# Kernel tuning notes

Measured on AMD Instinct MI355X. Metric: run time of the kernel, lower is better.

The kernel has to match this reference:

```python
import jax, jax.numpy as jnp
import numpy as np
from jax.scipy.special import erfinv

NEAR, FAR = 2.0, 6.0
NUM_COARSE, NUM_FINE = 128, 128
MAX_IPE_DEG = 16
REG_RED = 1.0            # cfg.train_params.reg_reduction_factor
SMOOTH = 2.0             # cfg.train_params.gaussian_smooth_factor
SQRT_2_OVER_PI = 0.7978845608028654


def approximate_cdf(x):
    # tanh approximation of the standard normal CDF (as in DDNeRF)
    return 0.5 * (1.0 + jnp.tanh(SQRT_2_OVER_PI * (x + 0.044715 * x ** 3)))


def cast_rays(t_vals, ro, rd, rr):
    # conical frustum -> diagonal gaussian (mip-NeRF)
    t0, t1 = t_vals[..., :-1], t_vals[..., 1:]
    c = 0.5 * (t0 + t1)
    d = 0.5 * (t1 - t0)
    denom = 3.0 * c ** 2 + d ** 2
    t_mean = c + (2.0 * c * d ** 2) / denom
    t_var = d ** 2 / 3.0 - (4.0 / 15.0) * (d ** 4 * (12.0 * c ** 2 - d ** 2)) / denom ** 2
    r_var = rr ** 2 * (c ** 2 / 4.0 + (5.0 / 12.0) * d ** 2 - (4.0 / 15.0) * d ** 4 / denom)
    mean = ro[..., None, :] + rd[..., None, :] * t_mean[..., None]          # [N,S,3]
    d2 = jnp.sum(rd ** 2, -1, keepdims=True)
    d_outer = rd ** 2
    null_outer = 1.0 - d_outer / jnp.maximum(d2, 1e-10)
    cov = t_var[..., None] * d_outer[..., None, :] + r_var[..., None] * null_outer[..., None, :]
    return mean, cov


def integrated_pos_enc(mean, cov):
    scales = 2.0 ** jnp.arange(MAX_IPE_DEG, dtype=mean.dtype)
    shp = mean.shape[:-1] + (MAX_IPE_DEG * 3,)
    y = (mean[..., None, :] * scales[:, None]).reshape(shp)
    yv = (cov[..., None, :] * scales[:, None] ** 2).reshape(shp)
    att = jnp.exp(-0.5 * yv)
    return jnp.concatenate([jnp.sin(y) * att, jnp.cos(y) * att], -1)        # [N,S,96]


def embed_dirs(d):
    # include_input=True, 4 log-sampled frequencies -> 3 + 24 = 27
    freqs = 2.0 ** jnp.arange(4, dtype=d.dtype)
    x = (d[..., None, :] * freqs[:, None]).reshape(d.shape[:-1] + (12,))
    return jnp.concatenate([d, jnp.sin(x), jnp.cos(x)], -1)


def mlp(enc, direnc, W0, b0, Wh, bh, Ws, bs, Wb, bb, Wd, bd, Wr, br, Wm=None, bm=None):
    x = jax.nn.relu(enc @ W0 + b0)
    for i in range(Wh.shape[0]):
        x = jax.nn.relu(x @ Wh[i] + bh[i])
    sigma = x @ Ws + bs                                                    # [N,S,1]
    bott = x @ Wb + bb
    de = jnp.broadcast_to(direnc[:, None, :], bott.shape[:-1] + (direnc.shape[-1],))
    h = jax.nn.relu(jnp.concatenate([bott, de], -1) @ Wd + bd)
    rgb = h @ Wr + br                                                      # [N,S,3]
    out = jnp.concatenate([rgb, sigma], -1)
    if Wm is not None:
        out = jnp.concatenate([out, x @ Wm + bm], -1)                      # + (mu, sig)
    return out


def volume_render(rf, t_vals, rd):
    rgb = jax.nn.sigmoid(rf[..., :3])
    sigma = jax.nn.relu(rf[..., 3])
    t0, t1 = t_vals[..., :-1], t_vals[..., 1:]
    dists = (t1 - t0) * jnp.linalg.norm(rd, axis=-1, keepdims=True)
    alpha = 1.0 - jnp.exp(-sigma * dists)
    trans = jnp.cumprod(1.0 - alpha + 1e-10, -1)
    trans = jnp.concatenate([jnp.ones_like(trans[..., :1]), trans[..., :-1]], -1)
    weights = alpha * trans
    rgb_map = jnp.sum(weights[..., None] * rgb, -2)
    t_mid = 0.5 * (t0 + t1)
    depth = jnp.sum(weights * t_mid, -1)
    acc = jnp.sum(weights, -1)
    return rgb_map, acc, weights, depth


def sample_pdf_mu_sigma(bins, weights, mus, sigmas, part_inside, left_tail, n_samples):
    # inverse-CDF sampling: outer categorical over bins, inner truncated gaussian in [0,1]
    w = weights + 1e-5
    pdf = w / jnp.sum(w, -1, keepdims=True)
    cdf = jnp.concatenate([jnp.zeros_like(pdf[..., :1]), jnp.cumsum(pdf, -1)], -1)
    u = jnp.linspace(0.0, 1.0 - 1e-5, n_samples, dtype=bins.dtype)
    u = jnp.broadcast_to(u, cdf.shape[:-1] + (n_samples,))
    idx = jax.vmap(lambda c, uu: jnp.searchsorted(c, uu, side='right'))(cdf, u) - 1
    idx = jnp.clip(idx, 0, pdf.shape[-1] - 1)
    g = lambda a: jnp.take_along_axis(a, idx, -1)
    frac = jnp.clip((u - g(cdf)) / jnp.maximum(g(pdf), 1e-10), 0.0, 1.0)
    p = jnp.clip(g(left_tail) + frac * g(part_inside), 1e-5, 1.0 - 1e-5)
    x = g(mus) + g(sigmas) * jnp.sqrt(2.0) * erfinv(2.0 * p - 1.0)
    x = jnp.clip(x, 0.0, 1.0)
    b0 = jnp.take_along_axis(bins, idx, -1)
    b1 = jnp.take_along_axis(bins, idx + 1, -1)
    return jnp.sort(b0 + x * (b1 - b0), -1)


def setup_inputs() -> dict:
    key = jax.random.key(0)
    ks = jax.random.split(key, 32)
    N = 2048
    d = {}
    d['ro'] = jax.random.normal(ks[0], (N, 3), jnp.float32)
    d['rd'] = jax.random.normal(ks[1], (N, 3), jnp.float32)
    d['rr'] = jax.random.uniform(ks[2], (N, 1), jnp.float32) * 0.01

    def w(k, shape):
        return jax.random.normal(k, shape, jnp.float32) * (1.0 / np.sqrt(shape[-2] if len(shape) > 1 else 1))

    for pfx, base in (('c', 3), ('f', 17)):
        d[pfx + 'W0'] = w(ks[base + 0], (96, 256));   d[pfx + 'b0'] = jnp.zeros((256,))
        d[pfx + 'Wh'] = w(ks[base + 1], (3, 256, 256)); d[pfx + 'bh'] = jnp.zeros((3, 256))
        d[pfx + 'Ws'] = w(ks[base + 2], (256, 1));    d[pfx + 'bs'] = jnp.zeros((1,))
        d[pfx + 'Wb'] = w(ks[base + 3], (256, 256));  d[pfx + 'bb'] = jnp.zeros((256,))
        d[pfx + 'Wd'] = w(ks[base + 4], (283, 128));  d[pfx + 'bd'] = jnp.zeros((128,))
        d[pfx + 'Wr'] = w(ks[base + 5], (128, 3));    d[pfx + 'br'] = jnp.zeros((3,))
    d['cWm'] = w(ks[10], (256, 2)); d['cbm'] = jnp.zeros((2,))
    return d


def reference(ro, rd, rr,
              cW0, cb0, cWh, cbh, cWs, cbs, cWb, cbb, cWd, cbd, cWr, cbr, cWm, cbm,
              fW0, fb0, fWh, fbh, fWs, fbs, fWb, fbb, fWd, fbd, fWr, fbr):
    N = ro.shape[0]
    viewdirs = rd / jnp.linalg.norm(rd, axis=-1, keepdims=True)
    direnc = embed_dirs(viewdirs)

    # ---- coarse pass (DepthMipNeRF: extra mu/sigma channels) ----
    t_vals = jnp.broadcast_to(jnp.linspace(NEAR, FAR, NUM_COARSE + 1, dtype=ro.dtype), (N, NUM_COARSE + 1))
    mean, cov = cast_rays(t_vals, ro, rd, rr)
    enc = integrated_pos_enc(mean, cov)
    rf = mlp(enc, direnc, cW0, cb0, cWh, cbh, cWs, cbs, cWb, cbb, cWd, cbd, cWr, cbr, cWm, cbm)
    raw_mus, raw_sig = rf[..., 4], rf[..., 5]
    mus = jax.nn.sigmoid(raw_mus / REG_RED)
    sigmas = jax.nn.sigmoid(raw_sig / REG_RED) + 0.001
    rgb_c, acc_c, weights, depth_c = volume_render(rf[..., :4], t_vals, rd)

    # smoothed per-bin truncated-gaussian stats
    sm_sig = sigmas * SMOOTH
    lt = approximate_cdf((0.0 - mus) / sm_sig)
    pib = approximate_cdf((1.0 - mus) / sm_sig) - lt

    # ---- fine pass ----
    t_fine = jax.lax.stop_gradient(
        sample_pdf_mu_sigma(t_vals, weights, mus, sm_sig, pib, lt, NUM_FINE + 1))
    mean, cov = cast_rays(t_fine, ro, rd, rr)
    enc = integrated_pos_enc(mean, cov)
    rf_f = mlp(enc, direnc, fW0, fb0, fWh, fbh, fWs, fbs, fWb, fbb, fWd, fbd, fWr, fbr)
    rgb_f, acc_f, w_f, depth_f = volume_render(rf_f, t_fine, rd)
    return rgb_c, rgb_f, depth_f, acc_f
```

## Files before the change

kernel.cpp:

```cpp
#include <hip/hip_runtime.h>

#define NRAYS 2048
#define LP 264

typedef _Float16 f16;
typedef __attribute__((ext_vector_type(4))) _Float16 f16x4;
typedef __attribute__((ext_vector_type(8))) _Float16 f16x8;
typedef __attribute__((ext_vector_type(4))) float f32x4;

__device__ __forceinline__ float sigmoidf(float x){ return 1.f/(1.f+expf(-x)); }

__device__ __forceinline__ float approx_cdf_f(float x){
  return 0.5f*(1.f + tanhf(0.7978845608028654f*(x + 0.044715f*x*x*x)));
}

__device__ __forceinline__ float erfinvf_dev(float x){
  float w = -logf((1.0f-x)*(1.0f+x));
  float p;
  if (w < 5.0f){
    w -= 2.5f;
    p = 2.81022636e-08f;
    p = fmaf(p,w, 3.43273939e-07f);
    p = fmaf(p,w,-3.5233877e-06f);
    p = fmaf(p,w,-4.39150654e-06f);
    p = fmaf(p,w, 0.00021858087f);
    p = fmaf(p,w,-0.00125372503f);
    p = fmaf(p,w,-0.00417768164f);
    p = fmaf(p,w, 0.246640727f);
    p = fmaf(p,w, 1.50140941f);
  } else {
    w = sqrtf(w) - 3.0f;
    p = -0.000200214257f;
    p = fmaf(p,w, 0.000100950558f);
    p = fmaf(p,w, 0.00134934322f);
    p = fmaf(p,w,-0.00367342844f);
    p = fmaf(p,w, 0.00573950773f);
    p = fmaf(p,w,-0.0076224613f);
    p = fmaf(p,w, 0.00943887047f);
    p = fmaf(p,w, 1.00167406f);
    p = fmaf(p,w, 2.83297682f);
  }
  return p*x;
}

__global__ void k_cvtT(const float* __restrict__ W, f16* __restrict__ Wh, f16* __restrict__ Wl,
                       int Ksrc, int N, int Kdst){
  int g = blockIdx.x*blockDim.x + threadIdx.x;
  if (g >= N*Kdst) return;
  int n = g / Kdst, k = g - n*Kdst;
  float v = (k < Ksrc) ? W[(size_t)k*N + n] : 0.f;
  f16 h = (f16)v;
  Wh[g] = h;
  Wl[g] = (f16)(v - (float)h);
}

struct Weights {
  const f16 *W0h,*W0l; const float *b0;
  const f16 *Whh,*Whl; const float *bh;
  const float *Ws,*bs,*Wm,*bm;
  const f16 *Wbh,*Wbl; const float *bb;
  const f16 *Wdh,*Wdl; const float *Wdfull,*bd;
  const float *Wr,*br;
};

template<int K, int N, bool SPLIT>
__device__ __forceinline__ void mlp_layer(
    f16* __restrict__ Xh, f16* __restrict__ Xl,
    const f16* __restrict__ Bh, const f16* __restrict__ Bl,
    const float* __restrict__ bias, const float* dctr, int relu,
    int wave, int q, int r)
{
  const int nbase = wave * 16;
  const bool act = (nbase < N);
  f32x4 acc[8];
  #pragma unroll
  for (int m=0;m<8;m++) acc[m] = (f32x4){0.f,0.f,0.f,0.f};
  if (act){
    const f16* bhp = Bh + (size_t)(nbase + r)*K + q*8;
    const f16* blp = Bl + (size_t)(nbase + r)*K + q*8;
    f16x8 bh = *(const f16x8*)bhp;
    f16x8 bl;
    if (SPLIT) bl = *(const f16x8*)blp;
    #pragma unroll
    for (int k0=0;k0<K;k0+=32){
      f16x8 bh_n, bl_n;
      if (k0+32 < K){
        bh_n = *(const f16x8*)(bhp + k0 + 32);
        if (SPLIT) bl_n = *(const f16x8*)(blp + k0 + 32);
      }
      #pragma unroll
      for (int m=0;m<8;m++){
        int ao = (m*16 + r)*LP + k0 + q*8;
        f16x8 ah = *(const f16x8*)&Xh[ao];
        acc[m] = __builtin_amdgcn_mfma_f32_16x16x32_f16(bh, ah, acc[m], 0,0,0);
        if (SPLIT){
          f16x8 al = *(const f16x8*)&Xl[ao];
          acc[m] = __builtin_amdgcn_mfma_f32_16x16x32_f16(bl, ah, acc[m], 0,0,0);
          acc[m] = __builtin_amdgcn_mfma_f32_16x16x32_f16(bh, al, acc[m], 0,0,0);
        }
      }
      bh = bh_n;
      if (SPLIT) bl = bl_n;
    }
  }
  __syncthreads();
  if (act){
    const int c0 = nbase + q*4;
    float ba0=0.f,ba1=0.f,ba2=0.f,ba3=0.f;
    if (bias){ ba0=bias[c0]; ba1=bias[c0+1]; ba2=bias[c0+2]; ba3=bias[c0+3]; }
    if (dctr){ ba0+=dctr[c0]; ba1+=dctr[c0+1]; ba2+=dctr[c0+2]; ba3+=dctr[c0+3]; }
    #pragma unroll
    for (int m=0;m<8;m++){
      int row = m*16 + r;
      float v0 = acc[m][0] + ba0, v1 = acc[m][1] + ba1;
      float v2 = acc[m][2] + ba2, v3 = acc[m][3] + ba3;
      if (relu){ v0=fmaxf(v0,0.f); v1=fmaxf(v1,0.f); v2=fmaxf(v2,0.f); v3=fmaxf(v3,0.f); }
      f16 h0=(f16)v0, h1=(f16)v1, h2=(f16)v2, h3=(f16)v3;
      f16x4 hv = {h0,h1,h2,h3};
      *(f16x4*)&Xh[row*LP + c0] = hv;
      if (SPLIT){
        f16x4 lv = {(f16)(v0-(float)h0),(f16)(v1-(float)h1),(f16)(v2-(float)h2),(f16)(v3-(float)h3)};
        *(f16x4*)&Xl[row*LP + c0] = lv;
      }
    }
  }
  __syncthreads();
}

__device__ __forceinline__ void enc_vals(
    float t0, float t1, float rrv,
    const float* rov, const float* rdv, float invdd,
    int j, int kk, float& a0, float& a1)
{
  float c = 0.5f*(t0+t1), d = 0.5f*(t1-t0);
  float c2 = c*c, d2 = d*d;
  float denom = 3.f*c2 + d2;
  float t_mean = c + 2.f*c*d2/denom;
  float d4 = d2*d2;
  float t_var = d2*(1.f/3.f) - (4.f/15.f)*(d4*(12.f*c2 - d2))/(denom*denom);
  float r_var = rrv*rrv*(c2*0.25f + (5.f/12.f)*d2 - (4.f/15.f)*d4/denom);
  float mean = rov[j] + rdv[j]*t_mean;
  float doj = rdv[j]*rdv[j];
  float cov = t_var*doj + r_var*(1.f - doj*invdd);
  float sc = (float)(1<<kk);
  float att = expf(-0.5f*cov*sc*sc);
  float sv, cv;
  sincosf(mean*sc, &sv, &cv);
  a0 = sv*att; a1 = cv*att;
}

__global__ __launch_bounds__(1024,4) void k_coarse(
    const float* __restrict__ ro, const float* __restrict__ rd, const float* __restrict__ rr,
    Weights w, float* __restrict__ tfine_out, float* __restrict__ dout)
{
  __shared__ f16 Xh[128*LP];
  __shared__ f16 Xl[128*LP];
  __shared__ float sh_de[32];
  __shared__ float sh_dctr[128];
  __shared__ float sh_sig[128], sh_mu[128], sh_sgm[128];
  __shared__ float sh_rgb[3*128];
  __shared__ float red[16];
  __shared__ float sh_w[128], sh_pdf[128], sh_cdf[132], sh_lt[128], sh_pib[128];
  __shared__ float s_wsum;

  int ray = blockIdx.x, tid = threadIdx.x;
  int wave = tid>>6, lane = tid&63, q = lane>>4, r = lane&15;

  float rdx = rd[ray*3], rdy = rd[ray*3+1], rdz = rd[ray*3+2];
  float rn = sqrtf(rdx*rdx+rdy*rdy+rdz*rdz);

  if (tid < 27){
    float v0=rdx/rn, v1=rdy/rn, v2=rdz/rn;
    float vv[3] = {v0,v1,v2};
    float o;
    if (tid < 3) o = vv[tid];
    else if (tid < 15){ int f=(tid-3)/3, j=(tid-3)%3; o = sinf(vv[j]*(float)(1<<f)); }
    else            { int f=(tid-15)/3, j=(tid-15)%3; o = cosf(vv[j]*(float)(1<<f)); }
    sh_de[tid] = o;
  }

  {
    int s = tid >> 3, p = tid & 7;
    float t0 = 2.f + 0.03125f*(float)s, t1 = t0 + 0.03125f;
    float rrv = rr[ray];
    float rdv[3] = {rdx, rdy, rdz};
    float rov[3] = {ro[ray*3], ro[ray*3+1], ro[ray*3+2]};
    float dd = rdx*rdx+rdy*rdy+rdz*rdz;
    float invdd = 1.f/fmaxf(dd, 1e-10f);
    #pragma unroll
    for (int j=0;j<3;j++){
      #pragma unroll
      for (int kk=p*2; kk<p*2+2; kk++){
        float a0, a1;
        enc_vals(t0,t1,rrv,rov,rdv,invdd,j,kk,a0,a1);
        f16 h0=(f16)a0, h1=(f16)a1;
        int i0 = s*LP + kk*3 + j, i1 = s*LP + 48 + kk*3 + j;
        Xh[i0]=h0; Xl[i0]=(f16)(a0-(float)h0);
        Xh[i1]=h1; Xl[i1]=(f16)(a1-(float)h1);
      }
    }
    #pragma unroll
    for (int i=0;i<4;i++){
      int col = 96 + p*4 + i;
      Xh[s*LP+col]=(f16)0.f; Xl[s*LP+col]=(f16)0.f;
    }
  }
  __syncthreads();

  if (tid < 128){
    float acc = w.bd[tid];
    #pragma unroll
    for (int k=0;k<27;k++) acc = fmaf(sh_de[k], w.Wdfull[(size_t)(256+k)*128 + tid], acc);
    sh_dctr[tid] = acc;
  }

  mlp_layer<128,256,true>(Xh,Xl, w.W0h, w.W0l, w.b0, nullptr, 1, wave,q,r);
  mlp_layer<256,256,true>(Xh,Xl, w.Whh,          w.Whl,          w.bh,      nullptr, 1, wave,q,r);
  mlp_layer<256,256,true>(Xh,Xl, w.Whh+65536,    w.Whl+65536,    w.bh+256,  nullptr, 1, wave,q,r);
  mlp_layer<256,256,true>(Xh,Xl, w.Whh+131072,   w.Whl+131072,   w.bh+512,  nullptr, 1, wave,q,r);

  {
    int row = tid>>3, p = tid&7;
    const f16* xh = &Xh[row*LP + p*32];
    const f16* xl = &Xl[row*LP + p*32];
    float s0=0.f, s1=0.f, s2=0.f;
    #pragma unroll
    for (int i=0;i<4;i++){
      f16x8 vh = *(const f16x8*)(xh + i*8);
      f16x8 vl = *(const f16x8*)(xl + i*8);
      #pragma unroll
      for (int e=0;e<8;e++){
        int k = p*32 + i*8 + e;
        float xv = (float)vh[e] + (float)vl[e];
        s0 = fmaf(xv, w.Ws[k], s0);
        s1 = fmaf(xv, w.Wm[2*k], s1);
        s2 = fmaf(xv, w.Wm[2*k+1], s2);
      }
    }
    s0 += __shfl_xor(s0,1); s0 += __shfl_xor(s0,2); s0 += __shfl_xor(s0,4);
    s1 += __shfl_xor(s1,1); s1 += __shfl_xor(s1,2); s1 += __shfl_xor(s1,4);
    s2 += __shfl_xor(s2,1); s2 += __shfl_xor(s2,2); s2 += __shfl_xor(s2,4);
    if (p==0){
      sh_sig[row] = s0 + w.bs[0];
      sh_mu[row]  = sigmoidf(s1 + w.bm[0]);
      sh_sgm[row] = 2.f*(sigmoidf(s2 + w.bm[1]) + 0.001f);
    }
  }

  mlp_layer<256,256,false>(Xh,Xl, w.Wbh, w.Wbl, w.bb, nullptr, 0, wave,q,r);
  mlp_layer<256,128,false>(Xh,Xl, w.Wdh, w.Wdl, nullptr, sh_dctr, 1, wave,q,r);

  {
    int row = tid>>3, p = tid&7;
    const f16* xh = &Xh[row*LP + p*16];
    float s0=0.f,s1=0.f,s2=0.f;
    #pragma unroll
    for (int i=0;i<2;i++){
      f16x8 vh = *(const f16x8*)(xh + i*8);
      #pragma unroll
      for (int e=0;e<8;e++){
        int k = p*16 + i*8 + e;
        float hv = (float)vh[e];
        s0 = fmaf(hv, w.Wr[3*k  ], s0);
        s1 = fmaf(hv, w.Wr[3*k+1], s1);
        s2 = fmaf(hv, w.Wr[3*k+2], s2);
      }
    }
    s0 += __shfl_xor(s0,1); s0 += __shfl_xor(s0,2); s0 += __shfl_xor(s0,4);
    s1 += __shfl_xor(s1,1); s1 += __shfl_xor(s1,2); s1 += __shfl_xor(s1,4);
    s2 += __shfl_xor(s2,1); s2 += __shfl_xor(s2,2); s2 += __shfl_xor(s2,4);
    if (p==0){
      sh_rgb[row*3  ] = s0 + w.br[0];
      sh_rgb[row*3+1] = s1 + w.br[1];
      sh_rgb[row*3+2] = s2 + w.br[2];
    }
  }
  __syncthreads();

  float alpha = 0.f;
  if (tid < 128){
    float sg = fmaxf(sh_sig[tid], 0.f);
    alpha = 1.f - expf(-sg * (0.03125f*rn));
    float mu = sh_mu[tid], sm = sh_sgm[tid];
    float lt = approx_cdf_f((0.f-mu)/sm);
    sh_lt[tid] = lt;
    sh_pib[tid] = approx_cdf_f((1.f-mu)/sm) - lt;
  }
  float incl = 1.f;
  if (tid < 128){
    incl = 1.f - alpha + 1e-10f;
    #pragma unroll
    for (int off=1; off<64; off<<=1){
      float y = __shfl_up(incl, off);
      if (lane >= off) incl *= y;
    }
    if (lane == 63) red[8 + (tid>>6)] = incl;
  }
  __syncthreads();
  if (tid < 128){
    float basep = (tid >= 64) ? red[8] : 1.f;
    float prev = __shfl_up(incl, 1);
    float excl = (lane == 0) ? 1.f : prev;
    sh_w[tid] = alpha * excl * basep;
  }
  __syncthreads();

  {
    float a0=0.f,a1=0.f,a2=0.f,a3=0.f;
    if (tid < 128){
      float wv = sh_w[tid];
      a0 = wv*sigmoidf(sh_rgb[tid*3+0]);
      a1 = wv*sigmoidf(sh_rgb[tid*3+1]);
      a2 = wv*sigmoidf(sh_rgb[tid*3+2]);
      a3 = wv + 1e-5f;
      #pragma unroll
      for (int off=32; off>0; off>>=1){
        a0 += __shfl_down(a0,off); a1 += __shfl_down(a1,off);
        a2 += __shfl_down(a2,off); a3 += __shfl_down(a3,off);
      }
      if (lane == 0){
        int wv2 = tid>>6;
        red[wv2*4+0]=a0; red[wv2*4+1]=a1; red[wv2*4+2]=a2; red[wv2*4+3]=a3;
      }
    }
    __syncthreads();
    if (tid==0){
      dout[ray*3  ] = red[0]+red[4];
      dout[ray*3+1] = red[1]+red[5];
      dout[ray*3+2] = red[2]+red[6];
      s_wsum = red[3]+red[7];
    }
  }
  __syncthreads();

  float aincl = 0.f;
  if (tid < 128){
    sh_pdf[tid] = (sh_w[tid]+1e-5f)/s_wsum;
    aincl = sh_pdf[tid];
    #pragma unroll
    for (int off=1; off<64; off<<=1){
      float y = __shfl_up(aincl, off);
      if (lane >= off) aincl += y;
    }
    if (lane == 63) red[12 + (tid>>6)] = aincl;
  }
  __syncthreads();
  if (tid < 128){
    float addp = (tid >= 64) ? red[12] : 0.f;
    sh_cdf[tid+1] = aincl + addp;
    if (tid == 0) sh_cdf[0] = 0.f;
  }
  __syncthreads();

  if (tid < 129){
    float u = (float)tid * ((1.f-1e-5f)/128.f);
    int lo=0, hi=129;
    while (lo<hi){ int mid=(lo+hi)>>1; if (sh_cdf[mid] <= u) lo=mid+1; else hi=mid; }
    int idx = lo-1; idx = idx<0?0:(idx>127?127:idx);
    float frac = (u - sh_cdf[idx]) / fmaxf(sh_pdf[idx], 1e-10f);
    frac = fminf(fmaxf(frac,0.f),1.f);
    float p = sh_lt[idx] + frac*sh_pib[idx];
    p = fminf(fmaxf(p, 1e-5f), 1.f-1e-5f);
    float xx = sh_mu[idx] + sh_sgm[idx]*1.4142135623730951f*erfinvf_dev(2.f*p-1.f);
    xx = fminf(fmaxf(xx,0.f),1.f);
    float b0 = 2.f + 0.03125f*(float)idx;
    tfine_out[(size_t)ray*129+tid] = b0 + xx*0.03125f;
  }
}

__global__ __launch_bounds__(1024,8) void k_fine(
    const float* __restrict__ ro, const float* __restrict__ rd, const float* __restrict__ rr,
    Weights w, const float* __restrict__ tfine_in, float* __restrict__ dout)
{
  __shared__ f16 Xh[128*LP];
  __shared__ float sh_t[132];
  __shared__ float sh_de[32];
  __shared__ float sh_dctr[128];
  __shared__ float sh_sig[128];
  __shared__ float sh_rgb[3*128];
  __shared__ float red[16];
  __shared__ float sh_w[128];

  int ray = blockIdx.x, tid = threadIdx.x;
  int wave = tid>>6, lane = tid&63, q = lane>>4, r = lane&15;

  float rdx = rd[ray*3], rdy = rd[ray*3+1], rdz = rd[ray*3+2];
  float rn = sqrtf(rdx*rdx+rdy*rdy+rdz*rdz);

  if (tid <= 128) sh_t[tid] = tfine_in[(size_t)ray*129 + tid];
  if (tid < 27){
    float v0=rdx/rn, v1=rdy/rn, v2=rdz/rn;
    float vv[3] = {v0,v1,v2};
    float o;
    if (tid < 3) o = vv[tid];
    else if (tid < 15){ int f=(tid-3)/3, j=(tid-3)%3; o = sinf(vv[j]*(float)(1<<f)); }
    else            { int f=(tid-15)/3, j=(tid-15)%3; o = cosf(vv[j]*(float)(1<<f)); }
    sh_de[tid] = o;
  }
  __syncthreads();

  {
    int s = tid >> 3, p = tid & 7;
    float t0 = sh_t[s], t1 = sh_t[s+1];
    float rrv = rr[ray];
    float rdv[3] = {rdx, rdy, rdz};
    float rov[3] = {ro[ray*3], ro[ray*3+1], ro[ray*3+2]};
    float dd = rdx*rdx+rdy*rdy+rdz*rdz;
    float invdd = 1.f/fmaxf(dd, 1e-10f);
    #pragma unroll
    for (int j=0;j<3;j++){
      #pragma unroll
      for (int kk=p*2; kk<p*2+2; kk++){
        float a0, a1;
        enc_vals(t0,t1,rrv,rov,rdv,invdd,j,kk,a0,a1);
        Xh[s*LP + kk*3 + j]      = (f16)a0;
        Xh[s*LP + 48 + kk*3 + j] = (f16)a1;
      }
    }
    #pragma unroll
    for (int i=0;i<4;i++) Xh[s*LP + 96 + p*4 + i] = (f16)0.f;
  }
  __syncthreads();

  if (tid < 128){
    float acc = w.bd[tid];
    #pragma unroll
    for (int k=0;k<27;k++) acc = fmaf(sh_de[k], w.Wdfull[(size_t)(256+k)*128 + tid], acc);
    sh_dctr[tid] = acc;
  }

  mlp_layer<128,256,false>(Xh,nullptr, w.W0h, w.W0l, w.b0, nullptr, 1, wave,q,r);
  mlp_layer<256,256,false>(Xh,nullptr, w.Whh,          w.Whl,          w.bh,      nullptr, 1, wave,q,r);
  mlp_layer<256,256,false>(Xh,nullptr, w.Whh+65536,    w.Whl+65536,    w.bh+256,  nullptr, 1, wave,q,r);
  mlp_layer<256,256,false>(Xh,nullptr, w.Whh+131072,   w.Whl+131072,   w.bh+512,  nullptr, 1, wave,q,r);

  {
    int row = tid>>3, p = tid&7;
    const f16* xh = &Xh[row*LP + p*32];
    float s0=0.f;
    #pragma unroll
    for (int i=0;i<4;i++){
      f16x8 vh = *(const f16x8*)(xh + i*8);
      #pragma unroll
      for (int e=0;e<8;e++) s0 = fmaf((float)vh[e], w.Ws[p*32+i*8+e], s0);
    }
    s0 += __shfl_xor(s0,1); s0 += __shfl_xor(s0,2); s0 += __shfl_xor(s0,4);
    if (p==0) sh_sig[row] = s0 + w.bs[0];
  }

  mlp_layer<256,256,false>(Xh,nullptr, w.Wbh, w.Wbl, w.bb, nullptr, 0, wave,q,r);
  mlp_layer<256,128,false>(Xh,nullptr, w.Wdh, w.Wdl, nullptr, sh_dctr, 1, wave,q,r);

  {
    int row = tid>>3, p = tid&7;
    const f16* xh = &Xh[row*LP + p*16];
    float s0=0.f,s1=0.f,s2=0.f;
    #pragma unroll
    for (int i=0;i<2;i++){
      f16x8 vh = *(const f16x8*)(xh + i*8);
      #pragma unroll
      for (int e=0;e<8;e++){
        int k = p*16 + i*8 + e;
        float hv = (float)vh[e];
        s0 = fmaf(hv, w.Wr[3*k  ], s0);
        s1 = fmaf(hv, w.Wr[3*k+1], s1);
        s2 = fmaf(hv, w.Wr[3*k+2], s2);
      }
    }
    s0 += __shfl_xor(s0,1); s0 += __shfl_xor(s0,2); s0 += __shfl_xor(s0,4);
    s1 += __shfl_xor(s1,1); s1 += __shfl_xor(s1,2); s1 += __shfl_xor(s1,4);
    s2 += __shfl_xor(s2,1); s2 += __shfl_xor(s2,2); s2 += __shfl_xor(s2,4);
    if (p==0){
      sh_rgb[row*3  ] = s0 + w.br[0];
      sh_rgb[row*3+1] = s1 + w.br[1];
      sh_rgb[row*3+2] = s2 + w.br[2];
    }
  }
  __syncthreads();

  float alpha = 0.f;
  if (tid < 128){
    float sg = fmaxf(sh_sig[tid], 0.f);
    alpha = 1.f - expf(-sg*(sh_t[tid+1]-sh_t[tid])*rn);
  }
  float incl = 1.f;
  if (tid < 128){
    incl = 1.f - alpha + 1e-10f;
    #pragma unroll
    for (int off=1; off<64; off<<=1){
      float y = __shfl_up(incl, off);
      if (lane >= off) incl *= y;
    }
    if (lane == 63) red[8 + (tid>>6)] = incl;
  }
  __syncthreads();
  if (tid < 128){
    float basep = (tid >= 64) ? red[8] : 1.f;
    float prev = __shfl_up(incl, 1);
    float excl = (lane == 0) ? 1.f : prev;
    sh_w[tid] = alpha * excl * basep;
  }
  __syncthreads();

  {
    float a0=0.f,a1=0.f,a2=0.f,a3=0.f,a4=0.f;
    if (tid < 128){
      float wv = sh_w[tid];
      a0 = wv*sigmoidf(sh_rgb[tid*3+0]);
      a1 = wv*sigmoidf(sh_rgb[tid*3+1]);
      a2 = wv*sigmoidf(sh_rgb[tid*3+2]);
      a3 = wv*0.5f*(sh_t[tid]+sh_t[tid+1]);
      a4 = wv;
      #pragma unroll
      for (int off=32; off>0; off>>=1){
        a0 += __shfl_down(a0,off); a1 += __shfl_down(a1,off);
        a2 += __shfl_down(a2,off); a3 += __shfl_down(a3,off);
        a4 += __shfl_down(a4,off);
      }
      if (lane == 0){
        int wv2 = tid>>6;
        red[wv2*5+0]=a0; red[wv2*5+1]=a1; red[wv2*5+2]=a2; red[wv2*5+3]=a3; red[wv2*5+4]=a4;
      }
    }
    __syncthreads();
    if (tid==0){
      dout[NRAYS*3 + ray*3  ] = red[0]+red[5];
      dout[NRAYS*3 + ray*3+1] = red[1]+red[6];
      dout[NRAYS*3 + ray*3+2] = red[2]+red[7];
      dout[NRAYS*6 + ray] = red[3]+red[8];
      dout[NRAYS*7 + ray] = red[4]+red[9];
    }
  }
}

extern "C" void kernel_launch(void* const* d_in, const int* in_sizes, int n_in,
                              void* d_out, int out_size, void* d_ws, size_t ws_size,
                              hipStream_t stream) {
  const float* ro  = (const float*)d_in[0];
  const float* rd  = (const float*)d_in[1];
  const float* rr  = (const float*)d_in[2];
  const float* cW0 = (const float*)d_in[3];  const float* cb0 = (const float*)d_in[4];
  const float* cWh = (const float*)d_in[5];  const float* cbh = (const float*)d_in[6];
  const float* cWs = (const float*)d_in[7];  const float* cbs = (const float*)d_in[8];
  const float* cWb = (const float*)d_in[9];  const float* cbb = (const float*)d_in[10];
  const float* cWd = (const float*)d_in[11]; const float* cbd = (const float*)d_in[12];
  const float* cWr = (const float*)d_in[13]; const float* cbr = (const float*)d_in[14];
  int iWm = 27, ibm = 28, ifb = 15;
  if (n_in > 15 && in_sizes[15] == 512){ iWm = 15; ibm = 16; ifb = 17; }
  const float* fW0 = (const float*)d_in[ifb+0];  const float* fb0 = (const float*)d_in[ifb+1];
  const float* fWh = (const float*)d_in[ifb+2];  const float* fbh = (const float*)d_in[ifb+3];
  const float* fWs = (const float*)d_in[ifb+4];  const float* fbs = (const float*)d_in[ifb+5];
  const float* fWb = (const float*)d_in[ifb+6];  const float* fbb = (const float*)d_in[ifb+7];
  const float* fWd = (const float*)d_in[ifb+8];  const float* fbd = (const float*)d_in[ifb+9];
  const float* fWr = (const float*)d_in[ifb+10]; const float* fbr = (const float*)d_in[ifb+11];
  const float* cWm = (const float*)d_in[iWm];    const float* cbm = (const float*)d_in[ibm];

  char* base = (char*)d_ws;
  size_t off = 0;
  auto alloc = [&](size_t bytes)->void*{ off = (off+63) & ~(size_t)63; void* p = base+off; off += bytes; return p; };

  float* tfine = (float*)alloc((size_t)NRAYS*129*4);
  f16 *cW0h=(f16*)alloc((size_t)256*128*2), *cW0l=(f16*)alloc((size_t)256*128*2);
  f16 *cWhh=(f16*)alloc((size_t)3*256*256*2), *cWhl=(f16*)alloc((size_t)3*256*256*2);
  f16 *cWbh=(f16*)alloc((size_t)256*256*2), *cWbl=(f16*)alloc((size_t)256*256*2);
  f16 *cWdh=(f16*)alloc((size_t)128*256*2), *cWdl=(f16*)alloc((size_t)128*256*2);
  f16 *fW0h=(f16*)alloc((size_t)256*128*2), *fW0l=(f16*)alloc((size_t)256*128*2);
  f16 *fWhh=(f16*)alloc((size_t)3*256*256*2), *fWhl=(f16*)alloc((size_t)3*256*256*2);
  f16 *fWbh=(f16*)alloc((size_t)256*256*2), *fWbl=(f16*)alloc((size_t)256*256*2);
  f16 *fWdh=(f16*)alloc((size_t)128*256*2), *fWdl=(f16*)alloc((size_t)128*256*2);

  k_cvtT<<<(256*128+255)/256,256,0,stream>>>(cW0, cW0h, cW0l, 96, 256, 128);
  for (int i=0;i<3;i++)
    k_cvtT<<<(256*256+255)/256,256,0,stream>>>(cWh+(size_t)i*65536, cWhh+(size_t)i*65536, cWhl+(size_t)i*65536, 256, 256, 256);
  k_cvtT<<<(256*256+255)/256,256,0,stream>>>(cWb, cWbh, cWbl, 256, 256, 256);
  k_cvtT<<<(128*256+255)/256,256,0,stream>>>(cWd, cWdh, cWdl, 256, 128, 256);
  k_cvtT<<<(256*128+255)/256,256,0,stream>>>(fW0, fW0h, fW0l, 96, 256, 128);
  for (int i=0;i<3;i++)
    k_cvtT<<<(256*256+255)/256,256,0,stream>>>(fWh+(size_t)i*65536, fWhh+(size_t)i*65536, fWhl+(size_t)i*65536, 256, 256, 256);
  k_cvtT<<<(256*256+255)/256,256,0,stream>>>(fWb, fWbh, fWbl, 256, 256, 256);
  k_cvtT<<<(128*256+255)/256,256,0,stream>>>(fWd, fWdh, fWdl, 256, 128, 256);

  Weights wc = { cW0h,cW0l,cb0, cWhh,cWhl,cbh, cWs,cbs,cWm,cbm,
                 cWbh,cWbl,cbb, cWdh,cWdl,cWd,cbd, cWr,cbr };
  Weights wf = { fW0h,fW0l,fb0, fWhh,fWhl,fbh, fWs,fbs,nullptr,nullptr,
                 fWbh,fWbl,fbb, fWdh,fWdl,fWd,fbd, fWr,fbr };

  k_coarse<<<NRAYS,1024,0,stream>>>(ro, rd, rr, wc, tfine, (float*)d_out);
  k_fine  <<<NRAYS,1024,0,stream>>>(ro, rd, rr, wf, tfine, (float*)d_out);
}
```

Measured before the change: 897.9 us.

## Store activations in MFMA fragment-tiled LDS layout instead of padded row-major

Replaces the padded row-major activation buffer in shared memory (stride 264) with a tiled layout in which each 16x32 MFMA operand tile is contiguous and lane-ordered. Each lane then reads its f16x8 operand at lane*8 inside the tile, which gives linear conflict-free LDS reads and simpler address arithmetic in the inner MFMA loop. Dropping the padding also shrinks the shared buffer (32768 vs 33792 halves per array), which may help occupancy. The epilogue writes, the encoding stores and the head reductions are all remapped to the new layout. The narrow f16x4 epilogue stores and scalar encoding stores could now see different bank-conflict patterns.

```diff
diff --git a/kernel.cpp b/kernel.cpp
--- a/kernel.cpp
+++ b/kernel.cpp
@@ -1,7 +1,10 @@
 #include <hip/hip_runtime.h>
 
 #define NRAYS 2048
-#define LP 264
+#define XTILE(m,kt) ((((m)<<3)+(kt))<<9)
+__device__ __forceinline__ int xaddr(int row, int col){
+  return XTILE(row>>4, col>>5) + ((((col&31)>>3)<<4) + (row&15))*8 + (col&7);
+}
 
 typedef _Float16 f16;
 typedef __attribute__((ext_vector_type(4))) _Float16 f16x4;
@@ -68,7 +71,7 @@
     f16* __restrict__ Xh, f16* __restrict__ Xl,
     const f16* __restrict__ Bh, const f16* __restrict__ Bl,
     const float* __restrict__ bias, const float* dctr, int relu,
-    int wave, int q, int r)
+    int wave, int q, int r, int lane)
 {
   const int nbase = wave * 16;
   const bool act = (nbase < N);
@@ -83,6 +86,7 @@
     if (SPLIT) bl = *(const f16x8*)blp;
     #pragma unroll
     for (int k0=0;k0<K;k0+=32){
+      const int kt = k0 >> 5;
       f16x8 bh_n, bl_n;
       if (k0+32 < K){
         bh_n = *(const f16x8*)(bhp + k0 + 32);
@@ -90,7 +94,7 @@
       }
       #pragma unroll
       for (int m=0;m<8;m++){
-        int ao = (m*16 + r)*LP + k0 + q*8;
+        int ao = XTILE(m,kt) + (lane<<3);
         f16x8 ah = *(const f16x8*)&Xh[ao];
         acc[m] = __builtin_amdgcn_mfma_f32_16x16x32_f16(bh, ah, acc[m], 0,0,0);
         if (SPLIT){
@@ -106,21 +110,22 @@
   __syncthreads();
   if (act){
     const int c0 = nbase + q*4;
+    const int ktp = c0 >> 5, qp = (c0 & 31) >> 3, j0 = c0 & 7;
     float ba0=0.f,ba1=0.f,ba2=0.f,ba3=0.f;
     if (bias){ ba0=bias[c0]; ba1=bias[c0+1]; ba2=bias[c0+2]; ba3=bias[c0+3]; }
     if (dctr){ ba0+=dctr[c0]; ba1+=dctr[c0+1]; ba2+=dctr[c0+2]; ba3+=dctr[c0+3]; }
     #pragma unroll
     for (int m=0;m<8;m++){
-      int row = m*16 + r;
+      int ao = XTILE(m,ktp) + ((qp<<4) + r)*8 + j0;
       float v0 = acc[m][0] + ba0, v1 = acc[m][1] + ba1;
       float v2 = acc[m][2] + ba2, v3 = acc[m][3] + ba3;
       if (relu){ v0=fmaxf(v0,0.f); v1=fmaxf(v1,0.f); v2=fmaxf(v2,0.f); v3=fmaxf(v3,0.f); }
       f16 h0=(f16)v0, h1=(f16)v1, h2=(f16)v2, h3=(f16)v3;
       f16x4 hv = {h0,h1,h2,h3};
-      *(f16x4*)&Xh[row*LP + c0] = hv;
+      *(f16x4*)&Xh[ao] = hv;
       if (SPLIT){
         f16x4 lv = {(f16)(v0-(float)h0),(f16)(v1-(float)h1),(f16)(v2-(float)h2),(f16)(v3-(float)h3)};
-        *(f16x4*)&Xl[row*LP + c0] = lv;
+        *(f16x4*)&Xl[ao] = lv;
       }
     }
   }
@@ -153,8 +158,8 @@
     const float* __restrict__ ro, const float* __restrict__ rd, const float* __restrict__ rr,
     Weights w, float* __restrict__ tfine_out, float* __restrict__ dout)
 {
-  __shared__ f16 Xh[128*LP];
-  __shared__ f16 Xl[128*LP];
+  __shared__ f16 Xh[32768];
+  __shared__ f16 Xl[32768];
   __shared__ float sh_de[32];
   __shared__ float sh_dctr[128];
   __shared__ float sh_sig[128], sh_mu[128], sh_sgm[128];
@@ -194,15 +199,15 @@
         float a0, a1;
         enc_vals(t0,t1,rrv,rov,rdv,invdd,j,kk,a0,a1);
         f16 h0=(f16)a0, h1=(f16)a1;
-        int i0 = s*LP + kk*3 + j, i1 = s*LP + 48 + kk*3 + j;
+        int i0 = xaddr(s, kk*3 + j), i1 = xaddr(s, 48 + kk*3 + j);
         Xh[i0]=h0; Xl[i0]=(f16)(a0-(float)h0);
         Xh[i1]=h1; Xl[i1]=(f16)(a1-(float)h1);
       }
     }
     #pragma unroll
     for (int i=0;i<4;i++){
-      int col = 96 + p*4 + i;
-      Xh[s*LP+col]=(f16)0.f; Xl[s*LP+col]=(f16)0.f;
+      int a = xaddr(s, 96 + p*4 + i);
+      Xh[a]=(f16)0.f; Xl[a]=(f16)0.f;
     }
   }
   __syncthreads();
@@ -214,20 +219,20 @@
     sh_dctr[tid] = acc;
   }
 
-  mlp_layer<128,256,true>(Xh,Xl, w.W0h, w.W0l, w.b0, nullptr, 1, wave,q,r);
-  mlp_layer<256,256,true>(Xh,Xl, w.Whh,          w.Whl,          w.bh,      nullptr, 1, wave,q,r);
-  mlp_layer<256,256,true>(Xh,Xl, w.Whh+65536,    w.Whl+65536,    w.bh+256,  nullptr, 1, wave,q,r);
-  mlp_layer<256,256,true>(Xh,Xl, w.Whh+131072,   w.Whl+131072,   w.bh+512,  nullptr, 1, wave,q,r);
+  mlp_layer<128,256,true>(Xh,Xl, w.W0h, w.W0l, w.b0, nullptr, 1, wave,q,r,lane);
+  mlp_layer<256,256,true>(Xh,Xl, w.Whh,          w.Whl,          w.bh,      nullptr, 1, wave,q,r,lane);
+  mlp_layer<256,256,true>(Xh,Xl, w.Whh+65536,    w.Whl+65536,    w.bh+256,  nullptr, 1, wave,q,r,lane);
+  mlp_layer<256,256,true>(Xh,Xl, w.Whh+131072,   w.Whl+131072,   w.bh+512,  nullptr, 1, wave,q,r,lane);
 
   {
     int row = tid>>3, p = tid&7;
-    const f16* xh = &Xh[row*LP + p*32];
-    const f16* xl = &Xl[row*LP + p*32];
+    int m = row>>4, rr_ = row&15;
     float s0=0.f, s1=0.f, s2=0.f;
     #pragma unroll
     for (int i=0;i<4;i++){
-      f16x8 vh = *(const f16x8*)(xh + i*8);
-      f16x8 vl = *(const f16x8*)(xl + i*8);
+      int a = XTILE(m,p) + ((i<<4) + rr_)*8;
+      f16x8 vh = *(const f16x8*)&Xh[a];
+      f16x8 vl = *(const f16x8*)&Xl[a];
       #pragma unroll
       for (int e=0;e<8;e++){
         int k = p*32 + i*8 + e;
@@ -247,16 +252,18 @@
     }
   }
 
-  mlp_layer<256,256,false>(Xh,Xl, w.Wbh, w.Wbl, w.bb, nullptr, 0, wave,q,r);
-  mlp_layer<256,128,false>(Xh,Xl, w.Wdh, w.Wdl, nullptr, sh_dctr, 1, wave,q,r);
+  mlp_layer<256,256,false>(Xh,Xl, w.Wbh, w.Wbl, w.bb, nullptr, 0, wave,q,r,lane);
+  mlp_layer<256,128,false>(Xh,Xl, w.Wdh, w.Wdl, nullptr, sh_dctr, 1, wave,q,r,lane);
 
   {
     int row = tid>>3, p = tid&7;
-    const f16* xh = &Xh[row*LP + p*16];
+    int m = row>>4, rr_ = row&15;
+    int kt = p>>1, qb = (p&1)*2;
     float s0=0.f,s1=0.f,s2=0.f;
     #pragma unroll
     for (int i=0;i<2;i++){
-      f16x8 vh = *(const f16x8*)(xh + i*8);
+      int a = XTILE(m,kt) + (((qb+i)<<4) + rr_)*8;
+      f16x8 vh = *(const f16x8*)&Xh[a];
       #pragma unroll
       for (int e=0;e<8;e++){
         int k = p*16 + i*8 + e;
@@ -372,7 +379,7 @@
     const float* __restrict__ ro, const float* __restrict__ rd, const float* __restrict__ rr,
     Weights w, const float* __restrict__ tfine_in, float* __restrict__ dout)
 {
-  __shared__ f16 Xh[128*LP];
+  __shared__ f16 Xh[32768];
   __shared__ float sh_t[132];
   __shared__ float sh_de[32];
   __shared__ float sh_dctr[128];
@@ -413,12 +420,12 @@
       for (int kk=p*2; kk<p*2+2; kk++){
         float a0, a1;
         enc_vals(t0,t1,rrv,rov,rdv,invdd,j,kk,a0,a1);
-        Xh[s*LP + kk*3 + j]      = (f16)a0;
-        Xh[s*LP + 48 + kk*3 + j] = (f16)a1;
-      }
-    }
-    #pragma unroll
-    for (int i=0;i<4;i++) Xh[s*LP + 96 + p*4 + i] = (f16)0.f;
+        Xh[xaddr(s, kk*3 + j)]      = (f16)a0;
+        Xh[xaddr(s, 48 + kk*3 + j)] = (f16)a1;
+      }
+    }
+    #pragma unroll
+    for (int i=0;i<4;i++) Xh[xaddr(s, 96 + p*4 + i)] = (f16)0.f;
   }
   __syncthreads();
 
@@ -429,18 +436,19 @@
     sh_dctr[tid] = acc;
   }
 
-  mlp_layer<128,256,false>(Xh,nullptr, w.W0h, w.W0l, w.b0, nullptr, 1, wave,q,r);
-  mlp_layer<256,256,false>(Xh,nullptr, w.Whh,          w.Whl,          w.bh,      nullptr, 1, wave,q,r);
-  mlp_layer<256,256,false>(Xh,nullptr, w.Whh+65536,    w.Whl+65536,    w.bh+256,  nullptr, 1, wave,q,r);
-  mlp_layer<256,256,false>(Xh,nullptr, w.Whh+131072,   w.Whl+131072,   w.bh+512,  nullptr, 1, wave,q,r);
+  mlp_layer<128,256,false>(Xh,nullptr, w.W0h, w.W0l, w.b0, nullptr, 1, wave,q,r,lane);
+  mlp_layer<256,256,false>(Xh,nullptr, w.Whh,          w.Whl,          w.bh,      nullptr, 1, wave,q,r,lane);
+  mlp_layer<256,256,false>(Xh,nullptr, w.Whh+65536,    w.Whl+65536,    w.bh+256,  nullptr, 1, wave,q,r,lane);
+  mlp_layer<256,256,false>(Xh,nullptr, w.Whh+131072,   w.Whl+131072,   w.bh+512,  nullptr, 1, wave,q,r,lane);
 
   {
     int row = tid>>3, p = tid&7;
-    const f16* xh = &Xh[row*LP + p*32];
+    int m = row>>4, rr_ = row&15;
     float s0=0.f;
     #pragma unroll
     for (int i=0;i<4;i++){
-      f16x8 vh = *(const f16x8*)(xh + i*8);
+      int a = XTILE(m,p) + ((i<<4) + rr_)*8;
+      f16x8 vh = *(const f16x8*)&Xh[a];
       #pragma unroll
       for (int e=0;e<8;e++) s0 = fmaf((float)vh[e], w.Ws[p*32+i*8+e], s0);
     }
@@ -448,16 +456,18 @@
     if (p==0) sh_sig[row] = s0 + w.bs[0];
   }
 
-  mlp_layer<256,256,false>(Xh,nullptr, w.Wbh, w.Wbl, w.bb, nullptr, 0, wave,q,r);
-  mlp_layer<256,128,false>(Xh,nullptr, w.Wdh, w.Wdl, nullptr, sh_dctr, 1, wave,q,r);
+  mlp_layer<256,256,false>(Xh,nullptr, w.Wbh, w.Wbl, w.bb, nullptr, 0, wave,q,r,lane);
+  mlp_layer<256,128,false>(Xh,nullptr, w.Wdh, w.Wdl, nullptr, sh_dctr, 1, wave,q,r,lane);
 
   {
     int row = tid>>3, p = tid&7;
-    const f16* xh = &Xh[row*LP + p*16];
+    int m = row>>4, rr_ = row&15;
+    int kt = p>>1, qb = (p&1)*2;
     float s0=0.f,s1=0.f,s2=0.f;
     #pragma unroll
     for (int i=0;i<2;i++){
-      f16x8 vh = *(const f16x8*)(xh + i*8);
+      int a = XTILE(m,kt) + (((qb+i)<<4) + rr_)*8;
+      f16x8 vh = *(const f16x8*)&Xh[a];
       #pragma unroll
       for (int e=0;e<8;e++){
         int k = p*16 + i*8 + e;
```

Result: no change. 903.7 us (+0.6%).
